# Kernel tuning notes

Measured on AMD Instinct MI355X. Metric: run time of the kernel, lower is better.

Reference implementation:

```python
import jax, jax.numpy as jnp
import numpy as np

DIM = 2048
HQ = 32
HKV = 8
HEAD_DIM = DIM // HQ          # 64
GROUP = HQ // HKV             # 4 q-heads per kv-head
B, S = 2, 2048


def setup_inputs() -> dict:
    key = jax.random.key(0)
    ks = jax.random.split(key, 12)
    sc_in = 1.0 / np.sqrt(DIM)   # lecun_normal fan-in scaling
    inp = {
        "q": jax.random.normal(ks[0], (B, S, DIM), jnp.float32),
        "k": jax.random.normal(ks[1], (B, S, DIM), jnp.float32),
        "v": jax.random.normal(ks[2], (B, S, DIM), jnp.float32),
        # causal 0/1 mask: module computes scores -= 1/mask + 1, so 0 -> -inf (masked), 1 -> -2 (softmax-invariant shift)
        "mask": jnp.tril(jnp.ones((S, S), jnp.int32)),
        "Wq": jax.random.normal(ks[3], (DIM, HQ * HEAD_DIM), jnp.float32) * sc_in,
        "bq": jnp.zeros((HQ * HEAD_DIM,), jnp.float32),
        "Wk": jax.random.normal(ks[4], (DIM, HKV * HEAD_DIM), jnp.float32) * sc_in,
        "bk": jnp.zeros((HKV * HEAD_DIM,), jnp.float32),
        "Wv": jax.random.normal(ks[5], (DIM, HKV * HEAD_DIM), jnp.float32) * sc_in,
        "bv": jnp.zeros((HKV * HEAD_DIM,), jnp.float32),
        "Wo": jax.random.normal(ks[6], (DIM, DIM), jnp.float32) * (1.0 / np.sqrt(DIM)),
        "bo": jnp.zeros((DIM,), jnp.float32),
    }
    return inp


def reference(q, k, v, mask, Wq, bq, Wk, bk, Wv, bv, Wo, bo):
    b, s, _ = q.shape
    # projections -> per-head layout
    qx = (q @ Wq + bq).reshape(b, s, HKV, GROUP, HEAD_DIM)   # grouped q-heads
    kx = (k @ Wk + bk).reshape(b, s, HKV, HEAD_DIM)
    vx = (v @ Wv + bv).reshape(b, s, HKV, HEAD_DIM)
    # scores[b, h, g, i, j] = q_i . k_j ; same math as repeating kv heads GROUP times
    scores = jnp.einsum('bihgd,bjhd->bhgij', qx, kx) / jnp.sqrt(
        jnp.asarray(HEAD_DIM, qx.dtype))
    # module's masking: scores -= 1/mask + 1  (mask==0 -> -inf, mask==1 -> -2)
    scores = scores - (1.0 / mask.astype(scores.dtype) + 1.0)
    probs = jax.nn.softmax(scores, axis=-1)
    out = jnp.einsum('bhgij,bjhd->bihgd', probs, vx).reshape(b, s, DIM)
    out = out @ Wo + bo
    return out
```

## Files before the change

kernel.cpp:

```cpp
#include <hip/hip_runtime.h>

typedef unsigned short u16;
typedef unsigned int u32;
typedef __attribute__((ext_vector_type(8))) short short8v;
typedef __attribute__((ext_vector_type(4))) float f32x4;

#define DIM 2048
#define HQN 32
#define HKVN 8
#define HD 64
#define BB 2
#define SS 2048
#define MTOT (BB*SS)
#define NKV (HKVN*HD)
#define QSCL 0.18033688011112042f

__device__ __forceinline__ u16 f2bf(float f){
  u32 u = __float_as_uint(f);
  u += 0x7FFFu + ((u >> 16) & 1u);
  return (u16)(u >> 16);
}

__device__ __forceinline__ u32 cvtpk(float a, float b){
  u32 r; asm("v_cvt_pk_bf16_f32 %0, %1, %2" : "=v"(r) : "v"(a), "v"(b)); return r;
}

__device__ __forceinline__ void gload_lds16(const void* g, void* l){
  __builtin_amdgcn_global_load_lds((const __attribute__((address_space(1))) u32*)g,
                                   (__attribute__((address_space(3))) u32*)l, 16, 0, 0);
}

#define WAITVM_(N) asm volatile("s_waitcnt vmcnt(" #N ")" ::: "memory")
#define WAITVM(N) WAITVM_(N)
#define BARF()    do { asm volatile("" ::: "memory"); __builtin_amdgcn_s_barrier(); asm volatile("" ::: "memory"); } while(0)
#define MF(a,b,cc) __builtin_amdgcn_mfma_f32_16x16x32_bf16((a),(b),(cc),0,0,0)

__global__ __launch_bounds__(256) void cast3_kernel(const float4* __restrict__ q,
                                                    const float4* __restrict__ k,
                                                    const float4* __restrict__ v,
                                                    u16* __restrict__ qo,
                                                    u16* __restrict__ ko,
                                                    u16* __restrict__ vo, int n4){
  const int z = blockIdx.y;
  const float4* in = z==0 ? q : (z==1 ? k : v);
  u16* out = z==0 ? qo : (z==1 ? ko : vo);
  int i = blockIdx.x*256 + threadIdx.x;
  if (i < n4){
    float4 f = in[i];
    union { u16 s[4]; unsigned long long u; } r;
    r.s[0]=f2bf(f.x); r.s[1]=f2bf(f.y); r.s[2]=f2bf(f.z); r.s[3]=f2bf(f.w);
    *(unsigned long long*)(out + (size_t)i*4) = r.u;
  }
}

__global__ __launch_bounds__(256) void transpose4_kernel(const float* __restrict__ Wq,
                                                         const float* __restrict__ Wk,
                                                         const float* __restrict__ Wv,
                                                         const float* __restrict__ Wo,
                                                         u16* __restrict__ WqT,
                                                         u16* __restrict__ WkT,
                                                         u16* __restrict__ WvT,
                                                         u16* __restrict__ WoT){
  const int z = blockIdx.z;
  const float* W = z==0?Wq:(z==1?Wk:(z==2?Wv:Wo));
  u16* WT = z==0?WqT:(z==1?WkT:(z==2?WvT:WoT));
  const int N = (z==1||z==2) ? NKV : DIM;
  const int K = DIM;
  int n0 = blockIdx.x*32, k0 = blockIdx.y*32;
  if (n0 >= N) return;
  __shared__ float tile[32][33];
  int tx = threadIdx.x & 31, ty = threadIdx.x >> 5;
  #pragma unroll
  for (int i=0;i<4;i++){
    int kk = ty + i*8;
    tile[kk][tx] = W[(size_t)(k0+kk)*N + n0 + tx];
  }
  __syncthreads();
  #pragma unroll
  for (int i=0;i<4;i++){
    int n = ty + i*8;
    WT[(size_t)(n0+n)*K + k0 + tx] = f2bf(tile[tx][n]);
  }
}

__global__ __launch_bounds__(512, 1) void gemm_qkv_kernel(const u16* __restrict__ Aq,
                                                          const u16* __restrict__ Ak,
                                                          const u16* __restrict__ Av,
                                                          const u16* __restrict__ BT,
                                                          const float* __restrict__ bq,
                                                          const float* __restrict__ bk,
                                                          const float* __restrict__ bv,
                                                          u16* __restrict__ Qp,
                                                          u16* __restrict__ Kp,
                                                          u16* __restrict__ Vp){
  __shared__ __align__(16) u16 lds[65536];
  char* ldsb = (char*)lds;
  const int t = threadIdx.x, lane = t & 63, w = t >> 6;
  const int wm = w >> 2, wn = w & 3, g = lane >> 4, c = lane & 15;
  int bid = blockIdx.x;
  bid = (bid & 7)*24 + (bid >> 3);
  const int mt = bid / 12, nt = bid - mt*12;
  const int m0 = mt*256, n0 = nt*256;
  const int seg = (n0 >= 2560) ? 2 : (n0 >= 2048 ? 1 : 0);
  const u16* A = seg==0 ? Aq : (seg==1 ? Ak : Av);
  const float* bias = seg==0 ? bq : (seg==1 ? bk : bv);
  const int nbase = seg==0 ? 0 : (seg==1 ? 2048 : 2560);

  const int rA = t >> 3;
  const int kc = ((t & 7) ^ (rA & 7)) * 8;
  const u16* gA = A  + (size_t)(m0 + rA)*DIM + kc;
  const u16* gB = BT + (size_t)(n0 + ((rA>>5)<<6) + (rA & 31))*DIM + kc;

  const u32 ko0 = (u32)((g*16) ^ ((c&7)<<4));
  const u32 ko1 = (u32)((64 + g*16) ^ ((c&7)<<4));
  const u32 aoff = wm*8192 + c*128;
  const u32 boff = wn*4096 + c*128;

#define STGA_(PA, KT, ABASE) do{ \
    gload_lds16(gA + (size_t)(KT)*64 + (size_t)((PA)*64)*DIM,       ldsb + (ABASE) + (PA)*16384 + t*16); \
    gload_lds16(gA + (size_t)(KT)*64 + (size_t)((PA)*64+128)*DIM,   ldsb + (ABASE) + (PA)*16384 + 8192 + t*16); }while(0)
#define STGB_(PB, KT, BBASE) do{ \
    gload_lds16(gB + (size_t)(KT)*64 + (size_t)((PB)*32)*DIM,       ldsb + (BBASE) + (PB)*16384 + t*16); \
    gload_lds16(gB + (size_t)(KT)*64 + (size_t)((PB)*32+128)*DIM,   ldsb + (BBASE) + (PB)*16384 + 8192 + t*16); }while(0)
#define LD8(OFF) (*(const short8v*)(ldsb + (OFF)))

  const f32x4 fzero = {0.f,0.f,0.f,0.f};
  f32x4 acc[8][4];
  #pragma unroll
  for (int i=0;i<8;i++)
    #pragma unroll
    for (int j=0;j<4;j++) acc[i][j] = fzero;

#define RD_A(PABASE) do{ _Pragma("unroll") for (int q=0;q<4;q++){ \
    a_[q][0] = LD8((PABASE) + aoff + q*2048 + ko0); \
    a_[q][1] = LD8((PABASE) + aoff + q*2048 + ko1); } }while(0)
#define RD_B(DST, PBBASE) do{ _Pragma("unroll") for (int s=0;s<2;s++){ \
    DST[s][0] = LD8((PBBASE) + boff + s*2048 + ko0); \
    DST[s][1] = LD8((PBBASE) + boff + s*2048 + ko1); } }while(0)

#define MM16(BSRC, FM0, FN0) do{ __builtin_amdgcn_s_setprio(1); \
    _Pragma("unroll") for (int q=0;q<4;q++) \
      _Pragma("unroll") for (int s=0;s<2;s++){ \
        acc[(FM0)+q][(FN0)+s] = MF(a_[q][0], BSRC[s][0], acc[(FM0)+q][(FN0)+s]); \
        acc[(FM0)+q][(FN0)+s] = MF(a_[q][1], BSRC[s][1], acc[(FM0)+q][(FN0)+s]); } \
    __builtin_amdgcn_s_setprio(0); }while(0)

#define QSTEP(TT, CUR, DOSTG, TAIL) do{ \
    const u32 AC = (CUR)*32768,  BC2 = 65536 + (CUR)*32768; \
    const u32 AN = (CUR^1)*32768, BN2 = 65536 + (CUR^1)*32768; \
    short8v a_[4][2], b0_[2][2], b1_[2][2]; \
     \
    RD_A(AC); RD_B(b0_, BC2); \
    if (DOSTG) { STGA_(0, (TT)+1, AN); STGB_(0, (TT)+1, BN2); \
                 STGB_(1, (TT)+1, BN2); STGA_(1, (TT)+1, AN); } \
    MM16(b0_, 0, 0); \
    if (TAIL) { WAITVM(2); } else { WAITVM(10); } \
    BARF(); \
     \
    RD_B(b1_, BC2 + 16384); \
    MM16(b1_, 0, 2); \
    if (TAIL) { WAITVM(0); } else { WAITVM(8); } \
    BARF(); \
     \
    RD_A(AC + 16384); \
    MM16(b1_, 4, 2); \
    BARF(); \
     \
    MM16(b0_, 4, 0); \
    if (!TAIL) { WAITVM(4); } \
    BARF(); \
  }while(0)

  STGA_(0, 0, 0); STGB_(0, 0, 65536); STGB_(1, 0, 65536); STGA_(1, 0, 0);
  WAITVM(4);
  BARF();

  #pragma unroll 1
  for (int tt = 0; tt < 30; tt += 2){
    QSTEP(tt,   0, 1, 0);
    QSTEP(tt+1, 1, 1, 0);
  }
  QSTEP(30, 0, 1, 0);
  QSTEP(31, 1, 0, 1);
#undef QSTEP

  WAITVM(0);
  __syncthreads();

  u16* st = lds + w*8192;
  const float osc = (seg == 0) ? QSCL : 1.0f;
  if (seg == 2){
    #pragma unroll
    for (int fm=0; fm<8; fm++){
      #pragma unroll
      for (int fn=0; fn<4; fn++){
        float bvv = bias[n0 - nbase + wn*64 + fn*16 + c];
        int vbase = (fm>>1)*2048 + fn*512 + (g*16 + c)*8 + (fm&1)*4;
        *(u32*)&st[vbase]     = cvtpk(acc[fm][fn][0]+bvv, acc[fm][fn][1]+bvv);
        *(u32*)&st[vbase + 2] = cvtpk(acc[fm][fn][2]+bvv, acc[fm][fn][3]+bvv);
      }
    }
  } else {
    #pragma unroll
    for (int fm=0; fm<8; fm++){
      #pragma unroll
      for (int fn=0; fn<4; fn++){
        float bvv = bias[n0 - nbase + wn*64 + fn*16 + c];
        int sbase = (fm>>1)*2048 + ((fm&1)*2 + (fn>>1))*512 + (c>>2)*128 + (fn&1)*4 + (c&3);
        #pragma unroll
        for (int r=0; r<4; r++)
          st[sbase + (4*g + r)*8] = f2bf((acc[fm][fn][r] + bvv)*osc);
      }
    }
  }
  __syncthreads();
  {
    const int bb = m0 >> 11;
    const int st0 = ((m0 & 2047) >> 5) + wm*4;
    u16* dst;
    if (seg == 0)      dst = Qp + (((size_t)bb*HQN  + (n0>>6)        + wn) << 17);
    else if (seg == 1) dst = Kp + (((size_t)bb*HKVN + ((n0-2048)>>6) + wn) << 17);
    else               dst = Vp + (((size_t)bb*HKVN + ((n0-2560)>>6) + wn) << 17);
    dst += (size_t)st0*2048;
    #pragma unroll
    for (int i=0;i<16;i++)
      *(short8v*)(dst + lane*8 + i*512) = *(const short8v*)(st + lane*8 + i*512);
  }
#undef STGA_
#undef STGB_
#undef RD_A
#undef RD_B
#undef MM16
#undef LD8
}

__global__ __launch_bounds__(512, 1) void gemm_o_kernel(const u16* __restrict__ A,
                                                        const u16* __restrict__ BT,
                                                        const float* __restrict__ bias,
                                                        float* __restrict__ C){
  __shared__ __align__(16) u16 lds[49152];
  char* ldsb = (char*)lds;
  const int t = threadIdx.x, lane = t & 63, w = t >> 6;
  const int wm = w >> 2, wn = w & 3, g = lane >> 4, c = lane & 15;
  int bid = blockIdx.x;
  bid = (bid & 7)*32 + (bid >> 3);
  const int m0 = (bid >> 4)*256, n0 = (bid & 15)*128;

  const int rA = t >> 3;
  const int kc = ((t & 7) ^ (rA & 7)) * 8;
  const u16* gA = A  + (size_t)(m0 + rA)*DIM + kc;
  const u16* gB = BT + (size_t)(n0 + rA)*DIM + kc;

  const u32 ko0 = (u32)((g*16) ^ ((c&7)<<4));
  const u32 ko1 = (u32)((64 + g*16) ^ ((c&7)<<4));
  const u32 aoff = wm*8192 + c*128;
  const u32 boffo = wn*4096 + c*128;

#define STGA_(PA, KT, ABASE) do{ \
    gload_lds16(gA + (size_t)(KT)*64 + (size_t)((PA)*64)*DIM,       ldsb + (ABASE) + (PA)*16384 + t*16); \
    gload_lds16(gA + (size_t)(KT)*64 + (size_t)((PA)*64+128)*DIM,   ldsb + (ABASE) + (PA)*16384 + 8192 + t*16); }while(0)
#define STGB_O(KT, BBASE) do{ \
    gload_lds16(gB + (size_t)(KT)*64,                     ldsb + (BBASE) + t*16); \
    gload_lds16(gB + (size_t)(KT)*64 + (size_t)64*DIM,    ldsb + (BBASE) + 8192 + t*16); }while(0)
#define LD8(OFF) (*(const short8v*)(ldsb + (OFF)))

  const f32x4 fzero = {0.f,0.f,0.f,0.f};
  f32x4 acc[8][2];
  #pragma unroll
  for (int i=0;i<8;i++){ acc[i][0] = fzero; acc[i][1] = fzero; }

#define RD_A(PABASE) do{ _Pragma("unroll") for (int q=0;q<4;q++){ \
    a_[q][0] = LD8((PABASE) + aoff + q*2048 + ko0); \
    a_[q][1] = LD8((PABASE) + aoff + q*2048 + ko1); } }while(0)
#define RD_BO(BBASE) do{ _Pragma("unroll") for (int s=0;s<2;s++){ \
    b_[s][0] = LD8((BBASE) + boffo + s*2048 + ko0); \
    b_[s][1] = LD8((BBASE) + boffo + s*2048 + ko1); } }while(0)

#define MMO(FM0) do{ __builtin_amdgcn_s_setprio(1); \
    _Pragma("unroll") for (int q=0;q<4;q++) \
      _Pragma("unroll") for (int s=0;s<2;s++){ \
        acc[(FM0)+q][s] = MF(a_[q][0], b_[s][0], acc[(FM0)+q][s]); \
        acc[(FM0)+q][s] = MF(a_[q][1], b_[s][1], acc[(FM0)+q][s]); } \
    __builtin_amdgcn_s_setprio(0); }while(0)

#define OSTEP(TT, CUR, DOSTG, TAIL) do{ \
    const u32 AC = (CUR)*32768,  BC2 = 65536 + (CUR)*16384; \
    const u32 AN = (CUR^1)*32768, BN2 = 65536 + (CUR^1)*16384; \
    short8v a_[4][2], b_[2][2]; \
     \
    RD_A(AC); RD_BO(BC2); \
    if (DOSTG) { STGA_(0, (TT)+1, AN); STGB_O((TT)+1, BN2); STGA_(1, (TT)+1, AN); } \
    MMO(0); \
    if (TAIL) { WAITVM(0); } else { WAITVM(6); } \
    BARF(); \
     \
    RD_A(AC + 16384); \
    MMO(4); \
    if (!TAIL) { WAITVM(2); } \
    BARF(); \
  }while(0)

  STGA_(0, 0, 0); STGB_O(0, 65536); STGA_(1, 0, 0);
  WAITVM(2);
  BARF();

  #pragma unroll 1
  for (int tt = 0; tt < 30; tt += 2){
    OSTEP(tt,   0, 1, 0);
    OSTEP(tt+1, 1, 1, 0);
  }
  OSTEP(30, 0, 1, 0);
  OSTEP(31, 1, 0, 1);
#undef OSTEP

  #pragma unroll
  for (int fm=0; fm<8; fm++){
    #pragma unroll
    for (int s=0; s<2; s++){
      int n = n0 + wn*32 + s*16 + c;
      float bvv = bias[n];
      #pragma unroll
      for (int r=0; r<4; r++){
        int m = m0 + wm*128 + fm*16 + 4*g + r;
        C[(size_t)m*DIM + n] = acc[fm][s][r] + bvv;
      }
    }
  }
#undef STGA_
#undef STGB_O
#undef RD_A
#undef RD_BO
#undef MMO
#undef LD8
}

__global__ __launch_bounds__(256) void attn_kernel(const u16* __restrict__ Qp,
                                                   const u16* __restrict__ Kp,
                                                   const u16* __restrict__ Vp,
                                                   u16* __restrict__ Aout){
  const int bid = blockIdx.x;
  const int grp = bid & 15;
  const int T   = 63 - (bid >> 4);
  const int b   = grp >> 3;
  const int hkv = grp & 7;
  const int t = threadIdx.x;
  const int lane = t & 63, w = t >> 6;
  const int g = lane >> 4, c = lane & 15;
  const int hq = hkv*4 + w;

  __shared__ __align__(16) u16 ring[4][2][2048];

  const u16* Kb = Kp + (((size_t)b*HKVN + hkv) << 17);
  const u16* Vb = Vp + (((size_t)b*HKVN + hkv) << 17);
  const u16* Qb = Qp + (((size_t)b*HQN + hq) << 17);
  const f32x4 fzero = {0.f,0.f,0.f,0.f};

  short8v qf[2][2];
  {
    const u16* qs = Qb + (size_t)T*2048 + lane*8;
    qf[0][0] = *(const short8v*)(qs);
    qf[0][1] = *(const short8v*)(qs + 512);
    qf[1][0] = *(const short8v*)(qs + 1024);
    qf[1][1] = *(const short8v*)(qs + 1536);
  }
  float l_r[2] = {0.f, 0.f};
  f32x4 o[2][4];
  #pragma unroll
  for (int qi=0; qi<2; qi++)
    #pragma unroll
    for (int f=0; f<4; f++) o[qi][f] = fzero;

  #pragma unroll
  for (int s=0; s<3; s++){
    const int tc = s > T ? T : s;
    gload_lds16(Kb + (size_t)tc*2048 + t*8, &ring[s][0][t*8]);
    gload_lds16(Vb + (size_t)tc*2048 + t*8, &ring[s][1][t*8]);
  }

  for (int kt = 0; kt <= T; kt += 4){
    #pragma unroll
    for (int s4 = 0; s4 < 4; ++s4){
      const int kt_ = kt + s4;
      if (kt_ > T) break;
      WAITVM(4);
      BARF();
      short8v kf0 = *(const short8v*)&ring[s4][0][lane*8];
      short8v kf1 = *(const short8v*)&ring[s4][0][512 + lane*8];
      short8v kf2 = *(const short8v*)&ring[s4][0][1024 + lane*8];
      short8v kf3 = *(const short8v*)&ring[s4][0][1536 + lane*8];
      short8v vf0 = *(const short8v*)&ring[s4][1][lane*8];
      short8v vf1 = *(const short8v*)&ring[s4][1][512 + lane*8];
      short8v vf2 = *(const short8v*)&ring[s4][1][1024 + lane*8];
      short8v vf3 = *(const short8v*)&ring[s4][1][1536 + lane*8];
      {
        const int tc = (kt_+3) > T ? T : (kt_+3);
        const int sn = (s4+3) & 3;
        gload_lds16(Kb + (size_t)tc*2048 + t*8, &ring[sn][0][t*8]);
        gload_lds16(Vb + (size_t)tc*2048 + t*8, &ring[sn][1][t*8]);
      }
      const bool diag = (kt_ == T);
      #pragma unroll
      for (int qi=0; qi<2; qi++){
        f32x4 s0 = fzero, s1 = fzero;
        __builtin_amdgcn_s_setprio(1);
        s0 = MF(kf0, qf[qi][0], s0);
        s0 = MF(kf1, qf[qi][1], s0);
        s1 = MF(kf2, qf[qi][0], s1);
        s1 = MF(kf3, qf[qi][1], s1);
        __builtin_amdgcn_s_setprio(0);
        float p0[4], p1[4];
        #pragma unroll
        for (int r=0; r<4; r++){
          p0[r] = __builtin_amdgcn_exp2f(s0[r]);
          p1[r] = __builtin_amdgcn_exp2f(s1[r]);
        }
        if (diag){
          const int qloc = qi*16 + c;
          #pragma unroll
          for (int r=0; r<4; r++){
            if (4*g + r      > qloc) p0[r] = 0.f;
            if (16 + 4*g + r > qloc) p1[r] = 0.f;
          }
        }
        l_r[qi] += (p0[0]+p0[1]) + (p0[2]+p0[3]) + (p1[0]+p1[1]) + (p1[2]+p1[3]);
        union { u32 u[4]; short8v v; } pu;
        pu.u[0] = cvtpk(p0[0], p0[1]);
        pu.u[1] = cvtpk(p0[2], p0[3]);
        pu.u[2] = cvtpk(p1[0], p1[1]);
        pu.u[3] = cvtpk(p1[2], p1[3]);
        __builtin_amdgcn_s_setprio(1);
        o[qi][0] = MF(pu.v, vf0, o[qi][0]);
        o[qi][1] = MF(pu.v, vf1, o[qi][1]);
        o[qi][2] = MF(pu.v, vf2, o[qi][2]);
        o[qi][3] = MF(pu.v, vf3, o[qi][3]);
        __builtin_amdgcn_s_setprio(0);
      }
    }
  }

  #pragma unroll
  for (int qi=0; qi<2; qi++){
    float ls = l_r[qi];
    ls += __shfl_xor(ls, 16);
    ls += __shfl_xor(ls, 32);
    float li = 1.0f / ls;
    float lf[4];
    #pragma unroll
    for (int r=0; r<4; r++) lf[r] = __shfl(li, 4*g + r);
    #pragma unroll
    for (int f=0; f<4; f++){
      #pragma unroll
      for (int r=0; r<4; r++){
        int q = T*32 + qi*16 + 4*g + r;
        Aout[((size_t)b*SS + q)*DIM + hq*HD + f*16 + c] = f2bf(o[qi][f][r]*lf[r]);
      }
    }
  }
}

extern "C" void kernel_launch(void* const* d_in, const int* in_sizes, int n_in,
                              void* d_out, int out_size, void* d_ws, size_t ws_size,
                              hipStream_t stream){
  const float* q  = (const float*)d_in[0];
  const float* k  = (const float*)d_in[1];
  const float* v  = (const float*)d_in[2];
  const float* Wq = (const float*)d_in[4];
  const float* bq = (const float*)d_in[5];
  const float* Wk = (const float*)d_in[6];
  const float* bk = (const float*)d_in[7];
  const float* Wv = (const float*)d_in[8];
  const float* bv = (const float*)d_in[9];
  const float* Wo = (const float*)d_in[10];
  const float* bo = (const float*)d_in[11];
  float* out = (float*)d_out;

  char* ws = (char*)d_ws;
  u16* q_bf = (u16*)ws; ws += (size_t)MTOT*DIM*2;
  u16* k_bf = (u16*)ws; ws += (size_t)MTOT*DIM*2;
  u16* v_bf = (u16*)ws; ws += (size_t)MTOT*DIM*2;
  u16* WqT  = (u16*)ws; ws += (size_t)DIM*DIM*2;
  u16* WkT  = (u16*)ws; ws += (size_t)NKV*DIM*2;
  u16* WvT  = (u16*)ws; ws += (size_t)NKV*DIM*2;
  u16* WoT  = (u16*)ws; ws += (size_t)DIM*DIM*2;
  u16* Qp   = (u16*)ws; ws += (size_t)MTOT*DIM*2;
  u16* Kp   = (u16*)ws; ws += (size_t)MTOT*NKV*2;
  u16* Vp   = (u16*)ws; ws += (size_t)MTOT*NKV*2;
  u16* attn = (u16*)ws; ws += (size_t)MTOT*DIM*2;

  const int n4 = MTOT*DIM/4;
  cast3_kernel<<<dim3(n4/256, 3), 256, 0, stream>>>((const float4*)q, (const float4*)k,
                                                    (const float4*)v, q_bf, k_bf, v_bf, n4);
  transpose4_kernel<<<dim3(DIM/32, DIM/32, 4), 256, 0, stream>>>(Wq, Wk, Wv, Wo,
                                                                 WqT, WkT, WvT, WoT);
  gemm_qkv_kernel<<<192, 512, 0, stream>>>(q_bf, k_bf, v_bf, WqT,
                                           bq, bk, bv, Qp, Kp, Vp);
  attn_kernel<<<1024, 256, 0, stream>>>(Qp, Kp, Vp, attn);
  gemm_o_kernel<<<256, 512, 0, stream>>>(attn, WoT, bo, out);
}
```

Before: 192.2 us.

## Simplify GEMM K-loop to one barrier per step with full fragment prefetch

Both the QKV projection and output projection main loops drop their multi-phase schedule. That schedule interleaved LDS fragment reads, MFMA groups and partial vmcnt waits across several barriers per K tile. Each step now waits for all outstanding global-to-LDS loads and passes one barrier. It then reads every A and B fragment for the tile into registers, issues the next tile's global loads into the other buffer, and runs all MFMAs back to back. This cuts barrier count and synchronisation overhead, but it needs more live registers and may hide less global-load latency, since each step blocks on the full previous transfer.

New measurement: 188.3 us. -2.0%, faster.

```diff
diff --git a/kernel.cpp b/kernel.cpp
--- a/kernel.cpp
+++ b/kernel.cpp
@@ -131,60 +131,47 @@
     #pragma unroll
     for (int j=0;j<4;j++) acc[i][j] = fzero;
 
-#define RD_A(PABASE) do{ _Pragma("unroll") for (int q=0;q<4;q++){ \
-    a_[q][0] = LD8((PABASE) + aoff + q*2048 + ko0); \
-    a_[q][1] = LD8((PABASE) + aoff + q*2048 + ko1); } }while(0)
+#define RD_A(DST, PABASE) do{ _Pragma("unroll") for (int q=0;q<4;q++){ \
+    DST[q][0] = LD8((PABASE) + aoff + q*2048 + ko0); \
+    DST[q][1] = LD8((PABASE) + aoff + q*2048 + ko1); } }while(0)
 #define RD_B(DST, PBBASE) do{ _Pragma("unroll") for (int s=0;s<2;s++){ \
     DST[s][0] = LD8((PBBASE) + boff + s*2048 + ko0); \
     DST[s][1] = LD8((PBBASE) + boff + s*2048 + ko1); } }while(0)
 
-#define MM16(BSRC, FM0, FN0) do{ __builtin_amdgcn_s_setprio(1); \
+#define MM16(ASRC, BSRC, FM0, FN0) do{ __builtin_amdgcn_s_setprio(1); \
     _Pragma("unroll") for (int q=0;q<4;q++) \
       _Pragma("unroll") for (int s=0;s<2;s++){ \
-        acc[(FM0)+q][(FN0)+s] = MF(a_[q][0], BSRC[s][0], acc[(FM0)+q][(FN0)+s]); \
-        acc[(FM0)+q][(FN0)+s] = MF(a_[q][1], BSRC[s][1], acc[(FM0)+q][(FN0)+s]); } \
+        acc[(FM0)+q][(FN0)+s] = MF(ASRC[q][0], BSRC[s][0], acc[(FM0)+q][(FN0)+s]); \
+        acc[(FM0)+q][(FN0)+s] = MF(ASRC[q][1], BSRC[s][1], acc[(FM0)+q][(FN0)+s]); } \
     __builtin_amdgcn_s_setprio(0); }while(0)
 
-#define QSTEP(TT, CUR, DOSTG, TAIL) do{ \
+#define QSTEP(TT, CUR, DOSTG) do{ \
     const u32 AC = (CUR)*32768,  BC2 = 65536 + (CUR)*32768; \
     const u32 AN = (CUR^1)*32768, BN2 = 65536 + (CUR^1)*32768; \
-    short8v a_[4][2], b0_[2][2], b1_[2][2]; \
-     \
-    RD_A(AC); RD_B(b0_, BC2); \
-    if (DOSTG) { STGA_(0, (TT)+1, AN); STGB_(0, (TT)+1, BN2); \
-                 STGB_(1, (TT)+1, BN2); STGA_(1, (TT)+1, AN); } \
-    MM16(b0_, 0, 0); \
-    if (TAIL) { WAITVM(2); } else { WAITVM(10); } \
+    short8v a0_[4][2], a1_[4][2], b0_[2][2], b1_[2][2]; \
+    WAITVM(0); \
     BARF(); \
-     \
-    RD_B(b1_, BC2 + 16384); \
-    MM16(b1_, 0, 2); \
-    if (TAIL) { WAITVM(0); } else { WAITVM(8); } \
-    BARF(); \
-     \
-    RD_A(AC + 16384); \
-    MM16(b1_, 4, 2); \
-    BARF(); \
-     \
-    MM16(b0_, 4, 0); \
-    if (!TAIL) { WAITVM(4); } \
-    BARF(); \
+    RD_A(a0_, AC); RD_B(b0_, BC2); RD_B(b1_, BC2 + 16384); \
+    if (DOSTG){ STGA_(0, (TT)+1, AN); STGB_(0, (TT)+1, BN2); \
+                STGB_(1, (TT)+1, BN2); STGA_(1, (TT)+1, AN); } \
+    RD_A(a1_, AC + 16384); \
+    MM16(a0_, b0_, 0, 0); \
+    MM16(a0_, b1_, 0, 2); \
+    MM16(a1_, b1_, 4, 2); \
+    MM16(a1_, b0_, 4, 0); \
   }while(0)
 
   STGA_(0, 0, 0); STGB_(0, 0, 65536); STGB_(1, 0, 65536); STGA_(1, 0, 0);
-  WAITVM(4);
-  BARF();
 
   #pragma unroll 1
   for (int tt = 0; tt < 30; tt += 2){
-    QSTEP(tt,   0, 1, 0);
-    QSTEP(tt+1, 1, 1, 0);
-  }
-  QSTEP(30, 0, 1, 0);
-  QSTEP(31, 1, 0, 1);
+    QSTEP(tt,   0, 1);
+    QSTEP(tt+1, 1, 1);
+  }
+  QSTEP(30, 0, 1);
+  QSTEP(31, 1, 0);
 #undef QSTEP
 
-  WAITVM(0);
   __syncthreads();
 
   u16* st = lds + w*8192;
@@ -269,48 +256,42 @@
   #pragma unroll
   for (int i=0;i<8;i++){ acc[i][0] = fzero; acc[i][1] = fzero; }
 
-#define RD_A(PABASE) do{ _Pragma("unroll") for (int q=0;q<4;q++){ \
-    a_[q][0] = LD8((PABASE) + aoff + q*2048 + ko0); \
-    a_[q][1] = LD8((PABASE) + aoff + q*2048 + ko1); } }while(0)
-#define RD_BO(BBASE) do{ _Pragma("unroll") for (int s=0;s<2;s++){ \
-    b_[s][0] = LD8((BBASE) + boffo + s*2048 + ko0); \
-    b_[s][1] = LD8((BBASE) + boffo + s*2048 + ko1); } }while(0)
-
-#define MMO(FM0) do{ __builtin_amdgcn_s_setprio(1); \
+#define RD_A(DST, PABASE) do{ _Pragma("unroll") for (int q=0;q<4;q++){ \
+    DST[q][0] = LD8((PABASE) + aoff + q*2048 + ko0); \
+    DST[q][1] = LD8((PABASE) + aoff + q*2048 + ko1); } }while(0)
+#define RD_BO(DST, BBASE) do{ _Pragma("unroll") for (int s=0;s<2;s++){ \
+    DST[s][0] = LD8((BBASE) + boffo + s*2048 + ko0); \
+    DST[s][1] = LD8((BBASE) + boffo + s*2048 + ko1); } }while(0)
+
+#define MMO(ASRC, FM0) do{ __builtin_amdgcn_s_setprio(1); \
     _Pragma("unroll") for (int q=0;q<4;q++) \
       _Pragma("unroll") for (int s=0;s<2;s++){ \
-        acc[(FM0)+q][s] = MF(a_[q][0], b_[s][0], acc[(FM0)+q][s]); \
-        acc[(FM0)+q][s] = MF(a_[q][1], b_[s][1], acc[(FM0)+q][s]); } \
+        acc[(FM0)+q][s] = MF(ASRC[q][0], b_[s][0], acc[(FM0)+q][s]); \
+        acc[(FM0)+q][s] = MF(ASRC[q][1], b_[s][1], acc[(FM0)+q][s]); } \
     __builtin_amdgcn_s_setprio(0); }while(0)
 
-#define OSTEP(TT, CUR, DOSTG, TAIL) do{ \
+#define OSTEP(TT, CUR, DOSTG) do{ \
     const u32 AC = (CUR)*32768,  BC2 = 65536 + (CUR)*16384; \
     const u32 AN = (CUR^1)*32768, BN2 = 65536 + (CUR^1)*16384; \
-    short8v a_[4][2], b_[2][2]; \
-     \
-    RD_A(AC); RD_BO(BC2); \
-    if (DOSTG) { STGA_(0, (TT)+1, AN); STGB_O((TT)+1, BN2); STGA_(1, (TT)+1, AN); } \
-    MMO(0); \
-    if (TAIL) { WAITVM(0); } else { WAITVM(6); } \
+    short8v a0_[4][2], a1_[4][2], b_[2][2]; \
+    WAITVM(0); \
     BARF(); \
-     \
-    RD_A(AC + 16384); \
-    MMO(4); \
-    if (!TAIL) { WAITVM(2); } \
-    BARF(); \
+    RD_A(a0_, AC); RD_BO(b_, BC2); \
+    if (DOSTG){ STGA_(0, (TT)+1, AN); STGB_O((TT)+1, BN2); STGA_(1, (TT)+1, AN); } \
+    RD_A(a1_, AC + 16384); \
+    MMO(a0_, 0); \
+    MMO(a1_, 4); \
   }while(0)
 
   STGA_(0, 0, 0); STGB_O(0, 65536); STGA_(1, 0, 0);
-  WAITVM(2);
-  BARF();
 
   #pragma unroll 1
   for (int tt = 0; tt < 30; tt += 2){
-    OSTEP(tt,   0, 1, 0);
-    OSTEP(tt+1, 1, 1, 0);
-  }
-  OSTEP(30, 0, 1, 0);
-  OSTEP(31, 1, 0, 1);
+    OSTEP(tt,   0, 1);
+    OSTEP(tt+1, 1, 1);
+  }
+  OSTEP(30, 0, 1);
+  OSTEP(31, 1, 0);
 #undef OSTEP
 
   #pragma unroll
```
